# Kernel optimization log

Measured on AMD Instinct MI355X. Metric: run time of the kernel, lower is better.

Reference implementation:

```python
import jax, jax.numpy as jnp
import numpy as np

N_NODES = 50000
EMBED = 64
N_EDGES = 1250000
N_USERS = 25000
BATCH, K = 1024, 100


def setup_inputs() -> dict:
    key = jax.random.key(0)
    ks = jax.random.split(key, 8)
    stdv = 1.0 / np.sqrt(EMBED)
    emb = jax.random.uniform(ks[0], (N_NODES, EMBED), jnp.float32, -stdv, stdv)
    # nn.Linear default init: U(-1/sqrt(fan_in), 1/sqrt(fan_in))
    lim = 1.0 / np.sqrt(EMBED)
    W0 = jax.random.uniform(ks[1], (EMBED, EMBED), jnp.float32, -lim, lim)
    b0 = jax.random.uniform(ks[2], (EMBED,), jnp.float32, -lim, lim)
    W1 = jax.random.uniform(ks[3], (EMBED, EMBED), jnp.float32, -lim, lim)
    b1 = jax.random.uniform(ks[4], (EMBED,), jnp.float32, -lim, lim)
    src = jax.random.randint(ks[5], (N_EDGES,), 0, N_NODES, jnp.int32)
    dst = jax.random.randint(ks[6], (N_EDGES,), 0, N_NODES, jnp.int32)
    user_index = jax.random.randint(ks[7], (BATCH, K), 0, N_USERS, jnp.int32)
    item_index = jax.random.randint(jax.random.fold_in(key, 99), (BATCH, K), 0, N_NODES, jnp.int32)
    return {"embeddings": emb, "W0": W0, "b0": b0, "W1": W1, "b1": b1,
            "src": src, "dst": dst, "user_index": user_index, "item_index": item_index}


def _mean_aggregate(h, src, dst):
    # copy_src gather + mailbox mean: mean of src features over incoming edges per dst
    msg_sum = jax.ops.segment_sum(h[src], dst, num_segments=N_NODES)  # [N, D]
    deg = jax.ops.segment_sum(jnp.ones((src.shape[0],), h.dtype), dst, num_segments=N_NODES)
    return msg_sum / jnp.maximum(deg, 1.0)[:, None]


def reference(embeddings, W0, b0, W1, b1, src, dst, user_index, item_index):
    h = embeddings
    for W, b in ((W0, b0), (W1, b1)):
        agg = _mean_aggregate(h, src, dst)          # [N, D] mean mailbox
        h = jnp.tanh(agg @ W.T + b)                  # NodeUpdate: Linear + Tanh
    user = h[user_index]                             # [B, K, D]
    item = h[item_index]                             # [B, K, D]
    score = jnp.sum(user * item, axis=2)             # [B, K]
    return score
```

## Files before the change

### kernel.cpp

```cpp
#include <hip/hip_runtime.h>

#define N_NODES 50000
#define N_EDGES 1250000
#define EMBED 64
#define N_PAIRS (1024 * 100)
#define BSHIFT 7
#define BSIZE 128
#define NBUCK 391
#define CB 153
#define LDS_CAP 4096

__device__ inline float bf2f(unsigned short u) {
    return __uint_as_float(((unsigned)u) << 16);
}
__device__ inline unsigned short f2bf(float x) {
    unsigned u = __float_as_uint(x);
    u += 0x7FFF + ((u >> 16) & 1);
    return (unsigned short)(u >> 16);
}

__global__ __launch_bounds__(1024) void hist_kernel(const int* __restrict__ dst,
                                                    int* __restrict__ counts) {
    __shared__ int hl[NBUCK];
    int t = threadIdx.x, b = blockIdx.x;
    for (int i = t; i < NBUCK; i += 1024) hl[i] = 0;
    __syncthreads();
    #pragma unroll
    for (int rep = 0; rep < 2; ++rep) {
        int i4 = b * 2048 + rep * 1024 + t;
        if (i4 < N_EDGES / 4) {
            int4 d = ((const int4*)dst)[i4];
            atomicAdd(&hl[d.x >> BSHIFT], 1);
            atomicAdd(&hl[d.y >> BSHIFT], 1);
            atomicAdd(&hl[d.z >> BSHIFT], 1);
            atomicAdd(&hl[d.w >> BSHIFT], 1);
        }
    }
    __syncthreads();
    for (int i = t; i < NBUCK; i += 1024) counts[b * NBUCK + i] = hl[i];
}

__global__ __launch_bounds__(512) void prep_kernel(const int* __restrict__ counts,
                                                   int* __restrict__ offs,
                                                   int* __restrict__ base) {
    __shared__ int ws[8];
    int t = threadIdx.x, lane = t & 63, wid = t >> 6;
    int tot = 0;
    if (t < NBUCK)
        for (int b = 0; b < CB; ++b) tot += counts[b * NBUCK + t];
    int incl = tot;
    #pragma unroll
    for (int off = 1; off < 64; off <<= 1) {
        int o = __shfl_up(incl, off);
        if (lane >= off) incl += o;
    }
    if (lane == 63) ws[wid] = incl;
    __syncthreads();
    if (t < 8) {
        int x = ws[t];
        #pragma unroll
        for (int off = 1; off < 8; off <<= 1) {
            int o = __shfl_up(x, off);
            if (t >= off) x += o;
        }
        ws[t] = x;
    }
    __syncthreads();
    int ex = ((wid > 0) ? ws[wid - 1] : 0) + incl - tot;
    if (t < NBUCK) base[t] = ex;
    if (t == 0) base[NBUCK] = N_EDGES;
    if (t < NBUCK) {
        int run = ex;
        for (int b = 0; b < CB; ++b) {
            offs[b * NBUCK + t] = run;
            run += counts[b * NBUCK + t];
        }
    }
}

__global__ __launch_bounds__(1024) void scatter_kernel(const int* __restrict__ src,
                                                       const int* __restrict__ dst,
                                                       const int* __restrict__ offs,
                                                       unsigned int* __restrict__ pairs) {
    __shared__ int cur[NBUCK];
    int t = threadIdx.x, b = blockIdx.x;
    for (int i = t; i < NBUCK; i += 1024) cur[i] = offs[b * NBUCK + i];
    __syncthreads();
    #pragma unroll
    for (int rep = 0; rep < 2; ++rep) {
        int i4 = b * 2048 + rep * 1024 + t;
        if (i4 < N_EDGES / 4) {
            int4 s4 = ((const int4*)src)[i4];
            int4 d4 = ((const int4*)dst)[i4];
            int p;
            p = atomicAdd(&cur[d4.x >> BSHIFT], 1);
            pairs[p] = ((unsigned)(d4.x & (BSIZE - 1)) << 16) | (unsigned)s4.x;
            p = atomicAdd(&cur[d4.y >> BSHIFT], 1);
            pairs[p] = ((unsigned)(d4.y & (BSIZE - 1)) << 16) | (unsigned)s4.y;
            p = atomicAdd(&cur[d4.z >> BSHIFT], 1);
            pairs[p] = ((unsigned)(d4.z & (BSIZE - 1)) << 16) | (unsigned)s4.z;
            p = atomicAdd(&cur[d4.w >> BSHIFT], 1);
            pairs[p] = ((unsigned)(d4.w & (BSIZE - 1)) << 16) | (unsigned)s4.w;
        }
    }
}

__global__ __launch_bounds__(256) void bucketsort_kernel(const unsigned int* __restrict__ pairs,
                                                         const int* __restrict__ base,
                                                         int* __restrict__ row,
                                                         int* __restrict__ col) {
    __shared__ unsigned ebuf[LDS_CAP];
    __shared__ int staged[LDS_CAP];
    __shared__ int hist[BSIZE];
    __shared__ int cur[BSIZE];
    __shared__ int wtot;
    int k = blockIdx.x, t = threadIdx.x;
    int lane = t & 63, wid = t >> 6;
    int nstart = k * BSIZE;
    int nodes = min(BSIZE, N_NODES - nstart);
    int estart = base[k], eend = base[k + 1];
    int cnt = eend - estart;
    if (t < BSIZE) hist[t] = 0;
    __syncthreads();
    if (cnt <= LDS_CAP) {
        for (int i = t; i < cnt; i += 256) {
            unsigned w = pairs[estart + i];
            ebuf[i] = w;
            atomicAdd(&hist[w >> 16], 1);
        }
        __syncthreads();
        if (t < BSIZE) {
            int v = hist[t];
            int incl = v;
            #pragma unroll
            for (int off = 1; off < 64; off <<= 1) {
                int o = __shfl_up(incl, off);
                if (lane >= off) incl += o;
            }
            if (t == 63) wtot = incl;
            __syncthreads();
            int ex = incl - v + ((wid == 1) ? wtot : 0);
            cur[t] = ex;
            if (t < nodes) row[nstart + t] = estart + ex;
        } else {
            __syncthreads();
        }
        if (k == NBUCK - 1 && t == 0) row[N_NODES] = N_EDGES;
        __syncthreads();
        for (int i = t; i < cnt; i += 256) {
            unsigned w = ebuf[i];
            int pos = atomicAdd(&cur[w >> 16], 1);
            staged[pos] = (int)(w & 0xFFFFu);
        }
        __syncthreads();
        for (int i = t; i < cnt; i += 256) col[estart + i] = staged[i];
    } else {
        for (int i = t; i < cnt; i += 256)
            atomicAdd(&hist[pairs[estart + i] >> 16], 1);
        __syncthreads();
        if (t < BSIZE) {
            int v = hist[t];
            int incl = v;
            #pragma unroll
            for (int off = 1; off < 64; off <<= 1) {
                int o = __shfl_up(incl, off);
                if (lane >= off) incl += o;
            }
            if (t == 63) wtot = incl;
            __syncthreads();
            int ex = incl - v + ((wid == 1) ? wtot : 0);
            cur[t] = ex;
            if (t < nodes) row[nstart + t] = estart + ex;
        } else {
            __syncthreads();
        }
        if (k == NBUCK - 1 && t == 0) row[N_NODES] = N_EDGES;
        __syncthreads();
        for (int i = t; i < cnt; i += 256) {
            unsigned w = pairs[estart + i];
            int pos = atomicAdd(&cur[w >> 16], 1);
            col[estart + pos] = (int)(w & 0xFFFFu);
        }
    }
}

__global__ __launch_bounds__(256) void gemv_f32_kernel(const float* __restrict__ h,
                                                       const float* __restrict__ W,
                                                       unsigned short* __restrict__ g) {
    __shared__ float hL[64][64];
    __shared__ float Wl[64][65];
    int t = threadIdx.x;
    int nstart = blockIdx.x * 64;
    int lane = t & 63, wid = t >> 6;
    for (int i = t; i < 4096; i += 256) Wl[i & 63][i >> 6] = W[i];
    int nrem = min(64, N_NODES - nstart);
    for (int i = t; i < nrem * 16; i += 256)
        ((float4*)hL)[i] = ((const float4*)(h + (size_t)nstart * EMBED))[i];
    __syncthreads();
    for (int n = wid; n < nrem; n += 4) {
        float x = 0.f;
        #pragma unroll
        for (int d = 0; d < 64; ++d)
            x += hL[n][d] * Wl[d][lane];
        g[(size_t)(nstart + n) * EMBED + lane] = f2bf(x);
    }
}

__global__ __launch_bounds__(256) void gemv_bf16_kernel(const unsigned short* __restrict__ h,
                                                        const float* __restrict__ W,
                                                        unsigned short* __restrict__ g) {
    __shared__ float hL[64][64];
    __shared__ float Wl[64][65];
    int t = threadIdx.x;
    int nstart = blockIdx.x * 64;
    int lane = t & 63, wid = t >> 6;
    for (int i = t; i < 4096; i += 256) Wl[i & 63][i >> 6] = W[i];
    int nrem = min(64, N_NODES - nstart);
    for (int i = t; i < nrem * 16; i += 256) {
        ushort4 v = ((const ushort4*)(h + (size_t)nstart * EMBED))[i];
        int r = i >> 4, c = (i & 15) * 4;
        hL[r][c + 0] = bf2f(v.x);
        hL[r][c + 1] = bf2f(v.y);
        hL[r][c + 2] = bf2f(v.z);
        hL[r][c + 3] = bf2f(v.w);
    }
    __syncthreads();
    for (int n = wid; n < nrem; n += 4) {
        float x = 0.f;
        #pragma unroll
        for (int d = 0; d < 64; ++d)
            x += hL[n][d] * Wl[d][lane];
        g[(size_t)(nstart + n) * EMBED + lane] = f2bf(x);
    }
}

__global__ __launch_bounds__(256) void agg_kernel(const unsigned short* __restrict__ g,
                                                  const float* __restrict__ bias,
                                                  const int* __restrict__ row,
                                                  const int* __restrict__ col,
                                                  unsigned short* __restrict__ hout) {
    int t = threadIdx.x;
    int wid = t >> 6, lane = t & 63;
    int node = blockIdx.x * 4 + wid;
    int gg = lane >> 4, d16 = lane & 15;
    int start = row[node], end = row[node + 1];
    float4 bb = ((const float4*)bias)[d16];
    float4 acc = {0.f, 0.f, 0.f, 0.f};
    for (int e = start; e < end; e += 32) {
        #pragma unroll
        for (int k = 0; k < 8; ++k) {
            int ee = e + 4 * k + gg;
            if (ee < end) {
                int s = col[ee];
                ushort4 v = ((const ushort4*)(g + (size_t)s * EMBED))[d16];
                acc.x += bf2f(v.x);
                acc.y += bf2f(v.y);
                acc.z += bf2f(v.z);
                acc.w += bf2f(v.w);
            }
        }
    }
    #pragma unroll
    for (int off = 16; off < 64; off <<= 1) {
        acc.x += __shfl_xor(acc.x, off);
        acc.y += __shfl_xor(acc.y, off);
        acc.z += __shfl_xor(acc.z, off);
        acc.w += __shfl_xor(acc.w, off);
    }
    int dg = end - start;
    float inv = (dg > 0) ? 1.0f / (float)dg : 0.f;
    if (gg == 0) {
        ushort4 o;
        o.x = f2bf(tanhf(acc.x * inv + bb.x));
        o.y = f2bf(tanhf(acc.y * inv + bb.y));
        o.z = f2bf(tanhf(acc.z * inv + bb.z));
        o.w = f2bf(tanhf(acc.w * inv + bb.w));
        ((ushort4*)(hout + (size_t)node * EMBED))[d16] = o;
    }
}

__global__ __launch_bounds__(256) void score_kernel(const unsigned short* __restrict__ h,
                                                    const int* __restrict__ ui,
                                                    const int* __restrict__ ii,
                                                    float* __restrict__ out) {
    int t = threadIdx.x;
    int idx = blockIdx.x * 16 + (t >> 4);
    int d16 = t & 15;
    int u = ui[idx];
    int v = ii[idx];
    ushort4 a4 = ((const ushort4*)(h + (size_t)u * EMBED))[d16];
    ushort4 b4 = ((const ushort4*)(h + (size_t)v * EMBED))[d16];
    float p = bf2f(a4.x) * bf2f(b4.x) + bf2f(a4.y) * bf2f(b4.y) +
              bf2f(a4.z) * bf2f(b4.z) + bf2f(a4.w) * bf2f(b4.w);
    #pragma unroll
    for (int off = 8; off > 0; off >>= 1)
        p += __shfl_xor(p, off);
    if (d16 == 0) out[idx] = p;
}

extern "C" void kernel_launch(void* const* d_in, const int* in_sizes, int n_in,
                              void* d_out, int out_size, void* d_ws, size_t ws_size,
                              hipStream_t stream) {
    const float* emb = (const float*)d_in[0];
    const float* W0  = (const float*)d_in[1];
    const float* b0  = (const float*)d_in[2];
    const float* W1  = (const float*)d_in[3];
    const float* b1  = (const float*)d_in[4];
    const int* src   = (const int*)d_in[5];
    const int* dst   = (const int*)d_in[6];
    const int* ui    = (const int*)d_in[7];
    const int* ii    = (const int*)d_in[8];
    float* out = (float*)d_out;

    char* p = (char*)d_ws;
    auto alloc = [&](size_t bytes) {
        char* r = p;
        p += (bytes + 255) & ~(size_t)255;
        return r;
    };
    int* counts          = (int*)alloc(sizeof(int) * NBUCK * CB);
    int* offs            = (int*)alloc(sizeof(int) * NBUCK * CB);
    int* base            = (int*)alloc(sizeof(int) * (NBUCK + 1));
    int* row             = (int*)alloc(sizeof(int) * (N_NODES + 1));
    unsigned* pairs      = (unsigned*)alloc(sizeof(unsigned) * N_EDGES);
    int* col             = (int*)alloc(sizeof(int) * N_EDGES);
    unsigned short* gbuf = (unsigned short*)alloc(sizeof(unsigned short) * N_NODES * EMBED);
    unsigned short* hbuf = (unsigned short*)alloc(sizeof(unsigned short) * N_NODES * EMBED);

    hist_kernel<<<CB, 1024, 0, stream>>>(dst, counts);
    prep_kernel<<<1, 512, 0, stream>>>(counts, offs, base);
    scatter_kernel<<<CB, 1024, 0, stream>>>(src, dst, offs, pairs);
    bucketsort_kernel<<<NBUCK, 256, 0, stream>>>(pairs, base, row, col);
    gemv_f32_kernel<<<(N_NODES + 63) / 64, 256, 0, stream>>>(emb, W0, gbuf);
    agg_kernel<<<N_NODES / 4, 256, 0, stream>>>(gbuf, b0, row, col, hbuf);
    gemv_bf16_kernel<<<(N_NODES + 63) / 64, 256, 0, stream>>>(hbuf, W1, gbuf);
    agg_kernel<<<N_NODES / 4, 256, 0, stream>>>(gbuf, b1, row, col, hbuf);
    score_kernel<<<N_PAIRS / 16, 256, 0, stream>>>(hbuf, ui, ii, out);
}
```

Measured before the change: 252.4 us.

## Fuse bucket sort with first GEMV and transpose per-block count layout

Merges the bucket-sort kernel and the first float32 GEMV into one launch whose block index picks the role, so the two independent stages run side by side and one launch is saved. Shared memory is carved by hand so both roles fit in one allocation. The counts and offsets arrays are also transposed to bucket-major, which makes prep_kernel's serial per-bucket loops read contiguous rows. Prep's reads per thread are now strided across threads rather than coalesced, and the larger shared footprint of the fused kernel may lower occupancy for the GEMV blocks.

```diff
diff --git a/kernel.cpp b/kernel.cpp
--- a/kernel.cpp
+++ b/kernel.cpp
@@ -9,6 +9,7 @@
 #define NBUCK 391
 #define CB 153
 #define LDS_CAP 4096
+#define GEMV_BLKS ((N_NODES + 63) / 64)
 
 __device__ inline float bf2f(unsigned short u) {
     return __uint_as_float(((unsigned)u) << 16);
@@ -37,7 +38,7 @@
         }
     }
     __syncthreads();
-    for (int i = t; i < NBUCK; i += 1024) counts[b * NBUCK + i] = hl[i];
+    for (int i = t; i < NBUCK; i += 1024) counts[i * CB + b] = hl[i];
 }
 
 __global__ __launch_bounds__(512) void prep_kernel(const int* __restrict__ counts,
@@ -45,9 +46,10 @@
                                                    int* __restrict__ base) {
     __shared__ int ws[8];
     int t = threadIdx.x, lane = t & 63, wid = t >> 6;
+    const int* rowp = counts + (size_t)t * CB;
     int tot = 0;
     if (t < NBUCK)
-        for (int b = 0; b < CB; ++b) tot += counts[b * NBUCK + t];
+        for (int b = 0; b < CB; ++b) tot += rowp[b];
     int incl = tot;
     #pragma unroll
     for (int off = 1; off < 64; off <<= 1) {
@@ -71,9 +73,10 @@
     if (t == 0) base[NBUCK] = N_EDGES;
     if (t < NBUCK) {
         int run = ex;
+        int* orow = offs + (size_t)t * CB;
         for (int b = 0; b < CB; ++b) {
-            offs[b * NBUCK + t] = run;
-            run += counts[b * NBUCK + t];
+            orow[b] = run;
+            run += rowp[b];
         }
     }
 }
@@ -84,7 +87,7 @@
                                                        unsigned int* __restrict__ pairs) {
     __shared__ int cur[NBUCK];
     int t = threadIdx.x, b = blockIdx.x;
-    for (int i = t; i < NBUCK; i += 1024) cur[i] = offs[b * NBUCK + i];
+    for (int i = t; i < NBUCK; i += 1024) cur[i] = offs[i * CB + b];
     __syncthreads();
     #pragma unroll
     for (int rep = 0; rep < 2; ++rep) {
@@ -105,104 +108,107 @@
     }
 }
 
-__global__ __launch_bounds__(256) void bucketsort_kernel(const unsigned int* __restrict__ pairs,
-                                                         const int* __restrict__ base,
-                                                         int* __restrict__ row,
-                                                         int* __restrict__ col) {
-    __shared__ unsigned ebuf[LDS_CAP];
-    __shared__ int staged[LDS_CAP];
-    __shared__ int hist[BSIZE];
-    __shared__ int cur[BSIZE];
-    __shared__ int wtot;
-    int k = blockIdx.x, t = threadIdx.x;
-    int lane = t & 63, wid = t >> 6;
-    int nstart = k * BSIZE;
-    int nodes = min(BSIZE, N_NODES - nstart);
-    int estart = base[k], eend = base[k + 1];
-    int cnt = eend - estart;
-    if (t < BSIZE) hist[t] = 0;
-    __syncthreads();
-    if (cnt <= LDS_CAP) {
-        for (int i = t; i < cnt; i += 256) {
-            unsigned w = pairs[estart + i];
-            ebuf[i] = w;
-            atomicAdd(&hist[w >> 16], 1);
-        }
-        __syncthreads();
-        if (t < BSIZE) {
-            int v = hist[t];
-            int incl = v;
-            #pragma unroll
-            for (int off = 1; off < 64; off <<= 1) {
-                int o = __shfl_up(incl, off);
-                if (lane >= off) incl += o;
-            }
-            if (t == 63) wtot = incl;
-            __syncthreads();
-            int ex = incl - v + ((wid == 1) ? wtot : 0);
-            cur[t] = ex;
-            if (t < nodes) row[nstart + t] = estart + ex;
-        } else {
-            __syncthreads();
-        }
-        if (k == NBUCK - 1 && t == 0) row[N_NODES] = N_EDGES;
-        __syncthreads();
-        for (int i = t; i < cnt; i += 256) {
-            unsigned w = ebuf[i];
-            int pos = atomicAdd(&cur[w >> 16], 1);
-            staged[pos] = (int)(w & 0xFFFFu);
-        }
-        __syncthreads();
-        for (int i = t; i < cnt; i += 256) col[estart + i] = staged[i];
-    } else {
-        for (int i = t; i < cnt; i += 256)
-            atomicAdd(&hist[pairs[estart + i] >> 16], 1);
-        __syncthreads();
-        if (t < BSIZE) {
-            int v = hist[t];
-            int incl = v;
-            #pragma unroll
-            for (int off = 1; off < 64; off <<= 1) {
-                int o = __shfl_up(incl, off);
-                if (lane >= off) incl += o;
-            }
-            if (t == 63) wtot = incl;
-            __syncthreads();
-            int ex = incl - v + ((wid == 1) ? wtot : 0);
-            cur[t] = ex;
-            if (t < nodes) row[nstart + t] = estart + ex;
-        } else {
-            __syncthreads();
-        }
-        if (k == NBUCK - 1 && t == 0) row[N_NODES] = N_EDGES;
-        __syncthreads();
-        for (int i = t; i < cnt; i += 256) {
-            unsigned w = pairs[estart + i];
-            int pos = atomicAdd(&cur[w >> 16], 1);
-            col[estart + pos] = (int)(w & 0xFFFFu);
-        }
-    }
-}
-
-__global__ __launch_bounds__(256) void gemv_f32_kernel(const float* __restrict__ h,
+#define SMEM_BYTES 33808
+__global__ __launch_bounds__(256) void sortgemv_kernel(const unsigned int* __restrict__ pairs,
+                                                       const int* __restrict__ base,
+                                                       int* __restrict__ row,
+                                                       int* __restrict__ col,
+                                                       const float* __restrict__ emb,
                                                        const float* __restrict__ W,
                                                        unsigned short* __restrict__ g) {
-    __shared__ float hL[64][64];
-    __shared__ float Wl[64][65];
+    __shared__ __align__(16) char smem[SMEM_BYTES];
     int t = threadIdx.x;
-    int nstart = blockIdx.x * 64;
-    int lane = t & 63, wid = t >> 6;
-    for (int i = t; i < 4096; i += 256) Wl[i & 63][i >> 6] = W[i];
-    int nrem = min(64, N_NODES - nstart);
-    for (int i = t; i < nrem * 16; i += 256)
-        ((float4*)hL)[i] = ((const float4*)(h + (size_t)nstart * EMBED))[i];
-    __syncthreads();
-    for (int n = wid; n < nrem; n += 4) {
-        float x = 0.f;
-        #pragma unroll
-        for (int d = 0; d < 64; ++d)
-            x += hL[n][d] * Wl[d][lane];
-        g[(size_t)(nstart + n) * EMBED + lane] = f2bf(x);
+    if (blockIdx.x < NBUCK) {
+        unsigned* ebuf = (unsigned*)smem;
+        int* staged    = (int*)(smem + 16384);
+        int* hist      = (int*)(smem + 32768);
+        int* cur       = (int*)(smem + 33280);
+        int* wtot      = (int*)(smem + 33792);
+        int k = blockIdx.x;
+        int lane = t & 63, wid = t >> 6;
+        int nstart = k * BSIZE;
+        int nodes = min(BSIZE, N_NODES - nstart);
+        int estart = base[k], eend = base[k + 1];
+        int cnt = eend - estart;
+        if (t < BSIZE) hist[t] = 0;
+        __syncthreads();
+        if (cnt <= LDS_CAP) {
+            for (int i = t; i < cnt; i += 256) {
+                unsigned w = pairs[estart + i];
+                ebuf[i] = w;
+                atomicAdd(&hist[w >> 16], 1);
+            }
+            __syncthreads();
+            if (t < BSIZE) {
+                int v = hist[t];
+                int incl = v;
+                #pragma unroll
+                for (int off = 1; off < 64; off <<= 1) {
+                    int o = __shfl_up(incl, off);
+                    if (lane >= off) incl += o;
+                }
+                if (t == 63) *wtot = incl;
+                __syncthreads();
+                int ex = incl - v + ((wid == 1) ? *wtot : 0);
+                cur[t] = ex;
+                if (t < nodes) row[nstart + t] = estart + ex;
+            } else {
+                __syncthreads();
+            }
+            if (k == NBUCK - 1 && t == 0) row[N_NODES] = N_EDGES;
+            __syncthreads();
+            for (int i = t; i < cnt; i += 256) {
+                unsigned w = ebuf[i];
+                int pos = atomicAdd(&cur[w >> 16], 1);
+                staged[pos] = (int)(w & 0xFFFFu);
+            }
+            __syncthreads();
+            for (int i = t; i < cnt; i += 256) col[estart + i] = staged[i];
+        } else {
+            for (int i = t; i < cnt; i += 256)
+                atomicAdd(&hist[pairs[estart + i] >> 16], 1);
+            __syncthreads();
+            if (t < BSIZE) {
+                int v = hist[t];
+                int incl = v;
+                #pragma unroll
+                for (int off = 1; off < 64; off <<= 1) {
+                    int o = __shfl_up(incl, off);
+                    if (lane >= off) incl += o;
+                }
+                if (t == 63) *wtot = incl;
+                __syncthreads();
+                int ex = incl - v + ((wid == 1) ? *wtot : 0);
+                cur[t] = ex;
+                if (t < nodes) row[nstart + t] = estart + ex;
+            } else {
+                __syncthreads();
+            }
+            if (k == NBUCK - 1 && t == 0) row[N_NODES] = N_EDGES;
+            __syncthreads();
+            for (int i = t; i < cnt; i += 256) {
+                unsigned w = pairs[estart + i];
+                int pos = atomicAdd(&cur[w >> 16], 1);
+                col[estart + pos] = (int)(w & 0xFFFFu);
+            }
+        }
+    } else {
+        float (*hL)[64] = (float (*)[64])smem;
+        float (*Wl)[65] = (float (*)[65])(smem + 16384);
+        int nstart = (blockIdx.x - NBUCK) * 64;
+        int lane = t & 63, wid = t >> 6;
+        for (int i = t; i < 4096; i += 256) Wl[i & 63][i >> 6] = W[i];
+        int nrem = min(64, N_NODES - nstart);
+        for (int i = t; i < nrem * 16; i += 256)
+            ((float4*)hL)[i] = ((const float4*)(emb + (size_t)nstart * EMBED))[i];
+        __syncthreads();
+        for (int n = wid; n < nrem; n += 4) {
+            float x = 0.f;
+            #pragma unroll
+            for (int d = 0; d < 64; ++d)
+                x += hL[n][d] * Wl[d][lane];
+            g[(size_t)(nstart + n) * EMBED + lane] = f2bf(x);
+        }
     }
 }
 
@@ -330,10 +336,10 @@
     hist_kernel<<<CB, 1024, 0, stream>>>(dst, counts);
     prep_kernel<<<1, 512, 0, stream>>>(counts, offs, base);
     scatter_kernel<<<CB, 1024, 0, stream>>>(src, dst, offs, pairs);
-    bucketsort_kernel<<<NBUCK, 256, 0, stream>>>(pairs, base, row, col);
-    gemv_f32_kernel<<<(N_NODES + 63) / 64, 256, 0, stream>>>(emb, W0, gbuf);
+    sortgemv_kernel<<<NBUCK + GEMV_BLKS, 256, 0, stream>>>(pairs, base, row, col,
+                                                           emb, W0, gbuf);
     agg_kernel<<<N_NODES / 4, 256, 0, stream>>>(gbuf, b0, row, col, hbuf);
-    gemv_bf16_kernel<<<(N_NODES + 63) / 64, 256, 0, stream>>>(hbuf, W1, gbuf);
+    gemv_bf16_kernel<<<GEMV_BLKS, 256, 0, stream>>>(hbuf, W1, gbuf);
     agg_kernel<<<N_NODES / 4, 256, 0, stream>>>(gbuf, b1, row, col, hbuf);
     score_kernel<<<N_PAIRS / 16, 256, 0, stream>>>(hbuf, ui, ii, out);
 }
```

After: 257.7 us. 2.1% more time.
